# Kernel optimization log

Measured on AMD Instinct MI355X. Metric: run time of the kernel, lower is better.

The kernel has to match this reference:

```python
import jax, jax.numpy as jnp
import numpy as np

D_MODEL = 1024
N_HEADS = 16
DFF = 4096
B, S = 2, 2048
EPS = 1e-6


def _dense_params(key, d_in, d_out):
    kw, kb = jax.random.split(key)
    w = jax.random.normal(kw, (d_in, d_out), jnp.float32) * 0.02
    b = jax.random.normal(kb, (d_out,), jnp.float32) * 0.02
    return w, b


def setup_inputs() -> dict:
    key = jax.random.key(0)
    ks = jax.random.split(key, 20)
    inp = {
        "x": jax.random.normal(ks[0], (B, S, D_MODEL), jnp.float32),
        "enc_output": jax.random.normal(ks[1], (B, S, D_MODEL), jnp.float32),
        # causal look-ahead mask: 1 where attention is NOT allowed
        "look_ahead_mask": jnp.triu(jnp.ones((S, S), jnp.float32), k=1)[None, None],
        "padding_mask": (jax.random.uniform(ks[2], (B, 1, 1, S)) < 0.1).astype(jnp.float32),
    }
    names = ["mha1_wq", "mha1_wk", "mha1_wv", "mha1_wo",
             "mha2_wq", "mha2_wk", "mha2_wv", "mha2_wo"]
    for i, n in enumerate(names):
        w, b = _dense_params(ks[3 + i], D_MODEL, D_MODEL)
        inp[n] = w
        inp[n.replace("w", "b")] = b
    inp["ffn_w1"], inp["ffn_b1"] = _dense_params(ks[11], D_MODEL, DFF)
    inp["ffn_w2"], inp["ffn_b2"] = _dense_params(ks[12], DFF, D_MODEL)
    for i, n in enumerate(["ln1", "ln2", "ln3"]):
        inp[n + "_g"] = jnp.ones((D_MODEL,), jnp.float32)
        inp[n + "_b"] = jnp.zeros((D_MODEL,), jnp.float32)
    return inp


def _layernorm(x, g, b):
    mu = jnp.mean(x, axis=-1, keepdims=True)
    var = jnp.mean(jnp.square(x - mu), axis=-1, keepdims=True)
    return (x - mu) * jax.lax.rsqrt(var + EPS) * g + b


def _mha(v, k, q, mask, wq, bq, wk, bk, wv, bv, wo, bo):
    Bq, Sq, D = q.shape
    depth = D // N_HEADS

    def split(t):  # [B,S,D] -> [B,H,S,depth]
        return t.reshape(t.shape[0], -1, N_HEADS, depth).transpose(0, 2, 1, 3)

    qh = split(q @ wq + bq)
    kh = split(k @ wk + bk)
    vh = split(v @ wv + bv)
    logits = jnp.einsum("bhqd,bhkd->bhqk", qh, kh) / jnp.sqrt(jnp.float32(depth))
    if mask is not None:
        logits = logits + mask * (-1e9)
    attn = jax.nn.softmax(logits, axis=-1)
    out = jnp.einsum("bhqk,bhkd->bhqd", attn, vh)
    out = out.transpose(0, 2, 1, 3).reshape(Bq, Sq, D)
    return out @ wo + bo


def reference(x, enc_output, look_ahead_mask, padding_mask,
              mha1_wq, mha1_bq, mha1_wk, mha1_bk, mha1_wv, mha1_bv, mha1_wo, mha1_bo,
              mha2_wq, mha2_bq, mha2_wk, mha2_bk, mha2_wv, mha2_bv, mha2_wo, mha2_bo,
              ffn_w1, ffn_b1, ffn_w2, ffn_b2,
              ln1_g, ln1_b, ln2_g, ln2_b, ln3_g, ln3_b):
    # self-attention (training=False -> dropout is identity)
    attn1 = _mha(x, x, x, look_ahead_mask,
                 mha1_wq, mha1_bq, mha1_wk, mha1_bk, mha1_wv, mha1_bv, mha1_wo, mha1_bo)
    out1 = _layernorm(x + attn1, ln1_g, ln1_b)
    # cross-attention: q from decoder, k/v from encoder output
    attn2 = _mha(enc_output, enc_output, out1, padding_mask,
                 mha2_wq, mha2_bq, mha2_wk, mha2_bk, mha2_wv, mha2_bv, mha2_wo, mha2_bo)
    out2 = _layernorm(out1 + attn2, ln2_g, ln2_b)
    ffn = jax.nn.relu(out2 @ ffn_w1 + ffn_b1) @ ffn_w2 + ffn_b2
    return _layernorm(out2 + ffn, ln3_g, ln3_b)
```

## Files before the change

### kernel.cpp

```cpp
#include <hip/hip_runtime.h>
#include <hip/hip_bf16.h>
#include <stdint.h>

#define DM   1024
#define NH   16
#define SS   2048
#define BB   2
#define MT   4096

typedef __attribute__((ext_vector_type(8))) short short8;
typedef __attribute__((ext_vector_type(4))) float f32x4;

typedef __attribute__((address_space(1))) const unsigned int as1_uint;
typedef __attribute__((address_space(3))) unsigned int as3_uint;

__device__ __forceinline__ void async16(const void* g, void* l) {
  __builtin_amdgcn_global_load_lds((as1_uint*)g, (as3_uint*)l, 16, 0, 0);
}

#define WAITV(n) asm volatile("s_waitcnt vmcnt(" #n ")" ::: "memory")
#define BARRIER_SB() do { __builtin_amdgcn_s_barrier(); __builtin_amdgcn_sched_barrier(0); } while (0)
#define EXP2(x) __builtin_amdgcn_exp2f(x)

__device__ __forceinline__ unsigned short f2bf(float f) {
  union { float f; unsigned u; } c; c.f = f;
  unsigned r = c.u + 0x7fffu + ((c.u >> 16) & 1u);
  return (unsigned short)(r >> 16);
}

__device__ __forceinline__ unsigned cvt_pk_bf16(float lo, float hi) {
  unsigned r;
  asm("v_cvt_pk_bf16_f32 %0, %1, %2" : "=v"(r) : "v"(lo), "v"(hi));
  return r;
}

__device__ __forceinline__ float swz16(float x) {
  return __uint_as_float((unsigned)__builtin_amdgcn_ds_swizzle((int)__float_as_uint(x), 0x401F));
}

__global__ __launch_bounds__(256) void k_f32_to_bf16(
    const float* __restrict__ in, unsigned short* __restrict__ out, int n) {
  int i = (blockIdx.x * 256 + threadIdx.x) * 4;
  if (i >= n) return;
  float4 v = *(const float4*)(in + i);
  uint2 u;
  u.x = (unsigned)f2bf(v.x) | ((unsigned)f2bf(v.y) << 16);
  u.y = (unsigned)f2bf(v.z) | ((unsigned)f2bf(v.w) << 16);
  *(uint2*)(out + i) = u;
}

__global__ __launch_bounds__(256) void k_transpose_bf16(
    const float* __restrict__ in, unsigned short* __restrict__ out, int R, int C) {
  __shared__ float t[64][65];
  int c0 = blockIdx.x * 64, r0 = blockIdx.y * 64;
  int tx = threadIdx.x & 63, ty = threadIdx.x >> 6;
#pragma unroll
  for (int i = 0; i < 16; i++)
    t[ty + i * 4][tx] = in[(size_t)(r0 + ty + i * 4) * C + c0 + tx];
  __syncthreads();
#pragma unroll
  for (int i = 0; i < 16; i++)
    out[(size_t)(c0 + ty + i * 4) * R + r0 + tx] = f2bf(t[tx][ty + i * 4]);
}

template<int BM, int OUT_MODE, bool RELU, bool RESID, bool SPLITK>
__global__ __launch_bounds__(256) void k_gemm(
    const unsigned short* __restrict__ A,
    const unsigned short* __restrict__ Bt,
    const float* __restrict__ bias,
    const float* __restrict__ resid,
    void* __restrict__ outp, void* __restrict__ outp2,
    int M, int N, int K, int KS) {
  __shared__ unsigned short Alds[3][BM * 32];
  __shared__ unsigned short Blds[3][128 * 32];
  int tid = threadIdx.x;
  int w = tid >> 6, lane = tid & 63;
  int l15 = lane & 15, l4 = lane >> 4;
  int brow = blockIdx.y * BM, bcol = blockIdx.x * 128;

  constexpr int MR = 4;
  constexpr int NR = (BM == 128) ? 4 : 2;
  int wr = (BM == 128) ? (w >> 1) : 0;
  int wc = (BM == 128) ? (w & 1) : w;
  int rbase = wr * 64;
  int cbase = wc * (NR * 16);

  f32x4 acc[MR][NR];
#pragma unroll
  for (int i = 0; i < MR; i++)
#pragma unroll
    for (int j = 0; j < NR; j++) acc[i][j] = (f32x4){0.f, 0.f, 0.f, 0.f};

#define STAGEG(bufi, kk) do {                                                  \
    _Pragma("unroll")                                                          \
    for (int c = 0; c < BM / 64; c++) {                                        \
      int elem = (c * 256 + tid) * 8;                                          \
      int row = elem >> 5, col = elem & 31;                                    \
      async16(A + (size_t)(brow + row) * K + (kk) + col, &Alds[bufi][elem]);   \
    }                                                                          \
    _Pragma("unroll")                                                          \
    for (int c = 0; c < 2; c++) {                                              \
      int elem = (c * 256 + tid) * 8;                                          \
      int row = elem >> 5, col = elem & 31;                                    \
      async16(Bt + (size_t)(bcol + row) * K + (kk) + col, &Blds[bufi][elem]);  \
    } } while (0)

  int kbeg = SPLITK ? blockIdx.z * KS : 0;
  int nk = KS / 32;
  STAGEG(0, kbeg);
  if (nk > 1) {
    STAGEG(1, kbeg + 32);
    if (BM == 128) WAITV(4); else WAITV(3);
  } else {
    WAITV(0);
  }
  BARRIER_SB();

  for (int t = 0; t < nk; t++) {
    int buf = t % 3;
    if (t + 2 < nk) STAGEG((t + 2) % 3, kbeg + (t + 2) * 32);
    short8 af[MR], bfr[NR];
#pragma unroll
    for (int i = 0; i < MR; i++)
      af[i] = *(const short8*)&Alds[buf][(rbase + i * 16 + l15) * 32 + l4 * 8];
#pragma unroll
    for (int j = 0; j < NR; j++)
      bfr[j] = *(const short8*)&Blds[buf][(cbase + j * 16 + l15) * 32 + l4 * 8];
#pragma unroll
    for (int i = 0; i < MR; i++)
#pragma unroll
      for (int j = 0; j < NR; j++)
        acc[i][j] = __builtin_amdgcn_mfma_f32_16x16x32_bf16(af[i], bfr[j], acc[i][j], 0, 0, 0);
    if (t + 2 < nk) {
      if (BM == 128) WAITV(4); else WAITV(3);
    } else if (t + 1 < nk) {
      WAITV(0);
    }
    if (t + 1 < nk) BARRIER_SB();
  }
#undef STAGEG

  void* op = (SPLITK && blockIdx.z) ? outp2 : outp;
#pragma unroll
  for (int i = 0; i < MR; i++)
#pragma unroll
    for (int j = 0; j < NR; j++) {
      int row = brow + rbase + i * 16 + l4 * 4;
      int col = bcol + cbase + j * 16 + l15;
      float bs = (SPLITK || !bias) ? 0.f : bias[col];
#pragma unroll
      for (int r = 0; r < 4; r++) {
        float v = acc[i][j][r] + bs;
        if (RESID) v += resid[(size_t)(row + r) * N + col];
        if (RELU) v = fmaxf(v, 0.f);
        if (OUT_MODE == 0) ((float*)op)[(size_t)(row + r) * N + col] = v;
        else               ((unsigned short*)op)[(size_t)(row + r) * N + col] = f2bf(v);
      }
    }
}

__global__ __launch_bounds__(256) void k_gemm_qkv(
    const unsigned short* __restrict__ a0, const unsigned short* __restrict__ a1,
    const unsigned short* __restrict__ a2,
    const unsigned short* __restrict__ Bt,
    const float* __restrict__ b0, const float* __restrict__ b1, const float* __restrict__ b2,
    unsigned short* __restrict__ o0, unsigned short* __restrict__ o1, unsigned short* __restrict__ o2,
    int vmat, int M, int K) {
  __shared__ unsigned short Alds[3][128 * 32];
  __shared__ unsigned short Blds[3][128 * 32];
  int tid = threadIdx.x;
  int w = tid >> 6, lane = tid & 63;
  int wr = w >> 1, wc = w & 1;
  int l15 = lane & 15, l4 = lane >> 4;
  int z = blockIdx.z;
  const unsigned short* A  = (z == 0) ? a0 : (z == 1) ? a1 : a2;
  const unsigned short* Bz = Bt + (size_t)z * 1048576;
  int brow = blockIdx.y * 128, bcol = blockIdx.x * 128;

  f32x4 acc[4][4];
#pragma unroll
  for (int i = 0; i < 4; i++)
#pragma unroll
    for (int j = 0; j < 4; j++) acc[i][j] = (f32x4){0.f, 0.f, 0.f, 0.f};

#define STAGEQ(bufi, kk) do {                                                  \
    _Pragma("unroll")                                                          \
    for (int c = 0; c < 2; c++) {                                              \
      int elem = (c * 256 + tid) * 8;                                          \
      int row = elem >> 5, col = elem & 31;                                    \
      async16(A + (size_t)(brow + row) * K + (kk) + col, &Alds[bufi][elem]);   \
      async16(Bz + (size_t)(bcol + row) * K + (kk) + col, &Blds[bufi][elem]);  \
    } } while (0)

  int nk = K / 32;
  STAGEQ(0, 0);
  STAGEQ(1, 32);
  WAITV(4);
  BARRIER_SB();

  for (int t = 0; t < nk; t++) {
    int buf = t % 3;
    if (t + 2 < nk) STAGEQ((t + 2) % 3, (t + 2) * 32);
    short8 af[4], bfr[4];
#pragma unroll
    for (int i = 0; i < 4; i++) {
      af[i]  = *(const short8*)&Alds[buf][(wr * 64 + i * 16 + l15) * 32 + l4 * 8];
      bfr[i] = *(const short8*)&Blds[buf][(wc * 64 + i * 16 + l15) * 32 + l4 * 8];
    }
#pragma unroll
    for (int i = 0; i < 4; i++)
#pragma unroll
      for (int j = 0; j < 4; j++)
        acc[i][j] = __builtin_amdgcn_mfma_f32_16x16x32_bf16(af[i], bfr[j], acc[i][j], 0, 0, 0);
    if (t + 2 < nk) WAITV(4);
    else if (t + 1 < nk) WAITV(0);
    if (t + 1 < nk) BARRIER_SB();
  }
#undef STAGEQ

  const float* bias = (z == 0) ? b0 : (z == 1) ? b1 : b2;
  unsigned short* op = (z == 0) ? o0 : (z == 1) ? o1 : o2;
  bool tr = (z == vmat);
#pragma unroll
  for (int i = 0; i < 4; i++)
#pragma unroll
    for (int j = 0; j < 4; j++) {
      int row = brow + wr * 64 + i * 16 + l4 * 4;
      int colL = bcol + wc * 64 + j * 16 + l15;
      float bs = bias[colL];
#pragma unroll
      for (int r = 0; r < 4; r++) {
        float v = acc[i][j][r] + bs;
        if (tr) op[(size_t)colL * M + row + r] = f2bf(v);
        else    op[(size_t)(row + r) * 1024 + colL] = f2bf(v);
      }
    }
}

template<bool CAUSAL, int NF>
__global__ __launch_bounds__(256) void k_attn(
    const unsigned short* __restrict__ Q,
    const unsigned short* __restrict__ Kb,
    const unsigned short* __restrict__ Vt,
    const float* __restrict__ pm,
    unsigned short* __restrict__ out) {
  __shared__ unsigned short Klds[3][64 * 64];
  __shared__ unsigned short Vlds[3][64 * 64];
  __shared__ unsigned short Pw[4][NF][16 * 72];
  int tid = threadIdx.x, w = tid >> 6, lane = tid & 63;
  int l15 = lane & 15, l4 = lane >> 4;
  int h = blockIdx.y, b = blockIdx.z;
  const float SC = 0.125f * 1.44269504089f;
  const int NPASS = CAUSAL ? 2 : 1;

#define STAGE(bufi, kt_) do {                                                  \
    _Pragma("unroll")                                                          \
    for (int c = 0; c < 2; c++) {                                              \
      int e0 = w * 1024 + c * 512;                                             \
      int elem = e0 + lane * 8;                                                \
      int row_ = elem >> 6;                                                    \
      int col_ = (elem & 63) ^ ((row_ & 7) << 3);                              \
      async16(Kb + (size_t)(b * SS + (kt_) * 64 + row_) * DM + h * 64 + col_,  \
              &Klds[bufi][elem]);                                              \
      async16(Vt + (size_t)(h * 64 + row_) * MT + b * SS + (kt_) * 64 + col_,  \
              &Vlds[bufi][elem]);                                              \
    } } while (0)

  for (int pass = 0; pass < NPASS; pass++) {
    int qt = CAUSAL ? (pass == 0 ? (31 - (int)blockIdx.x) : (int)blockIdx.x)
                    : (int)blockIdx.x;
    int qbase = qt * (NF * 64) + w * (NF * 16);

    short8 qf[NF][2];
#pragma unroll
    for (int f = 0; f < NF; f++) {
      size_t qrow = (size_t)b * SS + qbase + f * 16 + l15;
#pragma unroll
      for (int ks = 0; ks < 2; ks++)
        qf[f][ks] = *(const short8*)(Q + qrow * DM + h * 64 + ks * 32 + l4 * 8);
    }

    float mrow[NF], lrow[NF];
    f32x4 accO[NF][4];
#pragma unroll
    for (int f = 0; f < NF; f++) {
      mrow[f] = -1e30f; lrow[f] = 0.f;
#pragma unroll
      for (int d = 0; d < 4; d++) accO[f][d] = (f32x4){0.f, 0.f, 0.f, 0.f};
    }

    int ktend = CAUSAL ? qt : (SS / 64 - 1);
    if (pass) BARRIER_SB();
    STAGE(0, 0);
    if (ktend >= 1) { STAGE(1, 1); WAITV(4); } else { WAITV(0); }
    BARRIER_SB();

    for (int kt = 0; kt <= ktend; kt++) {
      int buf = kt % 3;
      if (kt + 2 <= ktend) STAGE((kt + 2) % 3, kt + 2);

      bool active = !CAUSAL || (kt * 64 <= qbase + NF * 16 - 1);
      if (active) {
        f32x4 sa[NF][4];
#pragma unroll
        for (int f = 0; f < NF; f++)
#pragma unroll
          for (int nt = 0; nt < 4; nt++) sa[f][nt] = (f32x4){0.f, 0.f, 0.f, 0.f};
        __builtin_amdgcn_s_setprio(1);
#pragma unroll
        for (int ks = 0; ks < 2; ks++)
#pragma unroll
          for (int nt = 0; nt < 4; nt++) {
            int kr = nt * 16 + l15;
            short8 kf = *(const short8*)&Klds[buf][kr * 64 + ((ks * 32 + l4 * 8) ^ ((kr & 7) << 3))];
#pragma unroll
            for (int f = 0; f < NF; f++)
              sa[f][nt] = __builtin_amdgcn_mfma_f32_16x16x32_bf16(kf, qf[f][ks], sa[f][nt], 0, 0, 0);
          }
        __builtin_amdgcn_s_setprio(0);

        float pmb[16];
        if (!CAUSAL) {
#pragma unroll
          for (int nt = 0; nt < 4; nt++) {
            float4 pmv = *(const float4*)(pm + b * SS + kt * 64 + nt * 16 + l4 * 4);
#pragma unroll
            for (int r = 0; r < 4; r++) pmb[nt * 4 + r] = ((const float*)&pmv)[r] * -1e30f;
          }
        }
        bool diag = CAUSAL && (kt * 64 + 63 > qbase);

        float sv[NF][16], tm[NF];
#pragma unroll
        for (int f = 0; f < NF; f++) {
          if (CAUSAL && !diag) {
#pragma unroll
            for (int i = 0; i < 16; i++) sv[f][i] = sa[f][i >> 2][i & 3] * SC;
          } else if (CAUSAL) {
#pragma unroll
            for (int nt = 0; nt < 4; nt++)
#pragma unroll
              for (int r = 0; r < 4; r++) {
                float s = sa[f][nt][r] * SC;
                int kg = kt * 64 + nt * 16 + l4 * 4 + r;
                int qg = qbase + f * 16 + l15;
                if (kg > qg) s = -1e30f;
                sv[f][nt * 4 + r] = s;
              }
          } else {
#pragma unroll
            for (int i = 0; i < 16; i++)
              sv[f][i] = fmaf(sa[f][i >> 2][i & 3], SC, pmb[i]);
          }
          float t8[8];
#pragma unroll
          for (int i = 0; i < 8; i++) t8[i] = fmaxf(sv[f][i], sv[f][i + 8]);
#pragma unroll
          for (int i = 0; i < 4; i++) t8[i] = fmaxf(t8[i], t8[i + 4]);
          t8[0] = fmaxf(t8[0], t8[1]);
          t8[2] = fmaxf(t8[2], t8[3]);
          tm[f] = fmaxf(t8[0], t8[2]);
        }

        float sA[NF];
#pragma unroll
        for (int f = 0; f < NF; f++) sA[f] = swz16(tm[f]);
#pragma unroll
        for (int f = 0; f < NF; f++) tm[f] = fmaxf(tm[f], sA[f]);
        float xA[NF];
#pragma unroll
        for (int f = 0; f < NF; f++) xA[f] = __shfl_xor(tm[f], 32);
#pragma unroll
        for (int f = 0; f < NF; f++) tm[f] = fmaxf(tm[f], xA[f]);

#pragma unroll
        for (int f = 0; f < NF; f++) {
          if (!__all(tm[f] - mrow[f] <= 8.f)) {
            float mnew = fmaxf(mrow[f], tm[f]);
            float corr = EXP2(mrow[f] - mnew);
            mrow[f] = mnew;
            lrow[f] *= corr;
#pragma unroll
            for (int r = 0; r < 4; r++) {
              float cq = __shfl(corr, l4 * 4 + r);
#pragma unroll
              for (int dt = 0; dt < 4; dt++) accO[f][dt][r] *= cq;
            }
          }

          float p[16];
#pragma unroll
          for (int i = 0; i < 16; i++) p[i] = EXP2(sv[f][i] - mrow[f]);
          float a8[8];
#pragma unroll
          for (int i = 0; i < 8; i++) a8[i] = p[i] + p[i + 8];
#pragma unroll
          for (int i = 0; i < 4; i++) a8[i] = a8[i] + a8[i + 4];
          lrow[f] += (a8[0] + a8[1]) + (a8[2] + a8[3]);

#pragma unroll
          for (int nt = 0; nt < 4; nt++) {
            uint2 u;
            u.x = cvt_pk_bf16(p[nt * 4 + 0], p[nt * 4 + 1]);
            u.y = cvt_pk_bf16(p[nt * 4 + 2], p[nt * 4 + 3]);
            *(uint2*)&Pw[w][f][l15 * 72 + nt * 16 + l4 * 4] = u;
          }
        }

        __builtin_amdgcn_s_setprio(1);
#pragma unroll
        for (int ks = 0; ks < 2; ks++) {
          short8 pf[NF];
#pragma unroll
          for (int f = 0; f < NF; f++)
            pf[f] = *(const short8*)&Pw[w][f][l15 * 72 + ks * 32 + l4 * 8];
#pragma unroll
          for (int dt = 0; dt < 4; dt++) {
            int vr = dt * 16 + l15;
            short8 vf = *(const short8*)&Vlds[buf][vr * 64 + ((ks * 32 + l4 * 8) ^ ((vr & 7) << 3))];
#pragma unroll
            for (int f = 0; f < NF; f++)
              accO[f][dt] = __builtin_amdgcn_mfma_f32_16x16x32_bf16(pf[f], vf, accO[f][dt], 0, 0, 0);
          }
        }
        __builtin_amdgcn_s_setprio(0);
      }

      if (kt + 2 <= ktend) WAITV(4);
      else if (kt + 1 <= ktend) WAITV(0);
      if (kt + 1 <= ktend) BARRIER_SB();
    }

#pragma unroll
    for (int f = 0; f < NF; f++) {
      lrow[f] += swz16(lrow[f]);
      lrow[f] += __shfl_xor(lrow[f], 32);
    }
#pragma unroll
    for (int f = 0; f < NF; f++)
#pragma unroll
      for (int r = 0; r < 4; r++) {
        float lq = __shfl(lrow[f], l4 * 4 + r);
        float inv = 1.f / lq;
        size_t row = (size_t)b * SS + qbase + f * 16 + l4 * 4 + r;
#pragma unroll
        for (int dt = 0; dt < 4; dt++)
          out[row * DM + h * 64 + dt * 16 + l15] = f2bf(accO[f][dt][r] * inv);
      }
  }
#undef STAGE
}

__global__ __launch_bounds__(256) void k_ln(
    const float* __restrict__ in, const float* __restrict__ in2,
    const float* __restrict__ resid, const float* __restrict__ bias,
    const float* __restrict__ g, const float* __restrict__ bb,
    float* __restrict__ outf, unsigned short* __restrict__ outb) {
  int row = blockIdx.x, tid = threadIdx.x;
  int w = tid >> 6;
  __shared__ float red[4];
  float4 v = *(const float4*)(in + (size_t)row * 1024 + tid * 4);
  if (in2) {
    float4 v2 = *(const float4*)(in2 + (size_t)row * 1024 + tid * 4);
    v.x += v2.x; v.y += v2.y; v.z += v2.z; v.w += v2.w;
  }
  if (resid) {
    float4 v2 = *(const float4*)(resid + (size_t)row * 1024 + tid * 4);
    v.x += v2.x; v.y += v2.y; v.z += v2.z; v.w += v2.w;
  }
  if (bias) {
    float4 v2 = *(const float4*)(bias + tid * 4);
    v.x += v2.x; v.y += v2.y; v.z += v2.z; v.w += v2.w;
  }
  float s = v.x + v.y + v.z + v.w;
#pragma unroll
  for (int d = 1; d < 64; d <<= 1) s += __shfl_xor(s, d);
  if ((tid & 63) == 0) red[w] = s;
  __syncthreads();
  float mu = (red[0] + red[1] + red[2] + red[3]) * (1.f / 1024.f);
  float d0 = v.x - mu, d1 = v.y - mu, d2 = v.z - mu, d3 = v.w - mu;
  float q = d0 * d0 + d1 * d1 + d2 * d2 + d3 * d3;
#pragma unroll
  for (int d = 1; d < 64; d <<= 1) q += __shfl_xor(q, d);
  __syncthreads();
  if ((tid & 63) == 0) red[w] = q;
  __syncthreads();
  float var = (red[0] + red[1] + red[2] + red[3]) * (1.f / 1024.f);
  float rs = rsqrtf(var + 1e-6f);
  float4 gg = *(const float4*)(g + tid * 4);
  float4 bv = *(const float4*)(bb + tid * 4);
  float y0 = d0 * rs * gg.x + bv.x;
  float y1 = d1 * rs * gg.y + bv.y;
  float y2 = d2 * rs * gg.z + bv.z;
  float y3 = d3 * rs * gg.w + bv.w;
  if (outf) {
    float4 o; o.x = y0; o.y = y1; o.z = y2; o.w = y3;
    *(float4*)(outf + (size_t)row * 1024 + tid * 4) = o;
  }
  if (outb) {
    uint2 u;
    u.x = (unsigned)f2bf(y0) | ((unsigned)f2bf(y1) << 16);
    u.y = (unsigned)f2bf(y2) | ((unsigned)f2bf(y3) << 16);
    *(uint2*)(outb + (size_t)row * 1024 + tid * 4) = u;
  }
}

extern "C" void kernel_launch(void* const* d_in, const int* in_sizes, int n_in,
                              void* d_out, int out_size, void* d_ws, size_t ws_size,
                              hipStream_t stream) {
  const float* x    = (const float*)d_in[0];
  const float* enc  = (const float*)d_in[1];
  const float* pm   = (const float*)d_in[3];
  const float* wq1  = (const float*)d_in[4];   const float* bq1 = (const float*)d_in[5];
  const float* wk1  = (const float*)d_in[6];   const float* bk1 = (const float*)d_in[7];
  const float* wv1  = (const float*)d_in[8];   const float* bv1 = (const float*)d_in[9];
  const float* wo1  = (const float*)d_in[10];  const float* bo1 = (const float*)d_in[11];
  const float* wq2  = (const float*)d_in[12];  const float* bq2 = (const float*)d_in[13];
  const float* wk2  = (const float*)d_in[14];  const float* bk2 = (const float*)d_in[15];
  const float* wv2  = (const float*)d_in[16];  const float* bv2 = (const float*)d_in[17];
  const float* wo2  = (const float*)d_in[18];  const float* bo2 = (const float*)d_in[19];
  const float* fw1  = (const float*)d_in[20];  const float* fb1 = (const float*)d_in[21];
  const float* fw2  = (const float*)d_in[22];  const float* fb2 = (const float*)d_in[23];
  const float* ln1g = (const float*)d_in[24];  const float* ln1b = (const float*)d_in[25];
  const float* ln2g = (const float*)d_in[26];  const float* ln2b = (const float*)d_in[27];
  const float* ln3g = (const float*)d_in[28];  const float* ln3b = (const float*)d_in[29];

  char* ws = (char*)d_ws;
  unsigned short* XB = (unsigned short*)(ws + 0);
  unsigned short* EB = (unsigned short*)(ws + 8388608);
  unsigned short* Qb = (unsigned short*)(ws + 16777216);
  unsigned short* Kb = (unsigned short*)(ws + 25165824);
  unsigned short* Vt = (unsigned short*)(ws + 33554432);
  unsigned short* AT = (unsigned short*)(ws + 41943040);
  float*          T  = (float*)(ws + 50331648);
  float*          R  = (float*)(ws + 67108864);
  unsigned short* RB = (unsigned short*)(ws + 83886080);
  unsigned short* WT0 = (unsigned short*)(ws + 92274688);
  unsigned short* W1T = (unsigned short*)(ws + 92274688 + 16777216);
  unsigned short* W2T = (unsigned short*)(ws + 92274688 + 25165824);
  unsigned short* H   = (unsigned short*)(ws + 0);
  float*          T1  = (float*)(ws + 33554432);
  float*          T1o = (float*)(ws + 16777216);

  k_f32_to_bf16<<<4096, 256, 0, stream>>>(x, XB, MT * DM);
  k_f32_to_bf16<<<4096, 256, 0, stream>>>(enc, EB, MT * DM);
  const float* wlist[8] = {wq1, wk1, wv1, wo1, wq2, wk2, wv2, wo2};
  for (int i = 0; i < 8; i++)
    k_transpose_bf16<<<dim3(16, 16), 256, 0, stream>>>(wlist[i], WT0 + (size_t)i * 1048576, 1024, 1024);
  k_transpose_bf16<<<dim3(64, 16), 256, 0, stream>>>(fw1, W1T, 1024, 4096);
  k_transpose_bf16<<<dim3(16, 64), 256, 0, stream>>>(fw2, W2T, 4096, 1024);

  k_gemm_qkv<<<dim3(8, 32, 3), 256, 0, stream>>>(XB, XB, XB, WT0, bq1, bk1, bv1,
                                                 Qb, Kb, Vt, 2, MT, DM);
  k_attn<true, 1><<<dim3(16, 16, 2), 256, 0, stream>>>(Qb, Kb, Vt, nullptr, AT);
  k_gemm<64, 0, false, false, true><<<dim3(8, 64, 2), 256, 0, stream>>>(
      AT, WT0 + 3 * 1048576, nullptr, nullptr, T, T1o, MT, DM, DM, 512);
  k_ln<<<4096, 256, 0, stream>>>(T, T1o, x, bo1, ln1g, ln1b, R, RB);

  k_gemm_qkv<<<dim3(8, 32, 3), 256, 0, stream>>>(RB, EB, EB, WT0 + 4 * 1048576,
                                                 bq2, bk2, bv2, Qb, Kb, Vt, 2, MT, DM);
  k_attn<false, 2><<<dim3(16, 16, 2), 256, 0, stream>>>(Qb, Kb, Vt, pm, AT);
  k_gemm<64, 0, false, false, true><<<dim3(8, 64, 2), 256, 0, stream>>>(
      AT, WT0 + 7 * 1048576, nullptr, nullptr, T, T1o, MT, DM, DM, 512);
  k_ln<<<4096, 256, 0, stream>>>(T, T1o, R, bo2, ln2g, ln2b, R, RB);

  k_gemm<128, 1, true, false, false><<<dim3(32, 32), 256, 0, stream>>>(
      RB, W1T, fb1, nullptr, H, nullptr, MT, 4096, DM, 1024);
  k_gemm<64, 0, false, false, true><<<dim3(8, 64, 2), 256, 0, stream>>>(
      H, W2T, nullptr, nullptr, T, T1, MT, DM, 4096, 2048);
  k_ln<<<4096, 256, 0, stream>>>(T, T1, R, fb2, ln3g, ln3b, (float*)d_out, nullptr);
}
```

Baseline: 450.6 us.

## Batch conversion/transpose launches and add XCD-aware block swizzle to GEMMs

```diff
diff --git a/kernel.cpp b/kernel.cpp
--- a/kernel.cpp
+++ b/kernel.cpp
@@ -38,10 +38,24 @@
   return __uint_as_float((unsigned)__builtin_amdgcn_ds_swizzle((int)__float_as_uint(x), 0x401F));
 }
 
-__global__ __launch_bounds__(256) void k_f32_to_bf16(
-    const float* __restrict__ in, unsigned short* __restrict__ out, int n) {
-  int i = (blockIdx.x * 256 + threadIdx.x) * 4;
-  if (i >= n) return;
+__device__ __forceinline__ void xcd_swz(int& bx, int& by, int& bz) {
+  int GX = gridDim.x, GY = gridDim.y;
+  int nwg = GX * GY * gridDim.z;
+  int old = blockIdx.x + GX * (blockIdx.y + GY * blockIdx.z);
+  int f2 = (old & 7) * (nwg >> 3) + (old >> 3);
+  bz = f2 / (GX * GY);
+  int rem = f2 % (GX * GY);
+  bx = rem / GY;
+  by = rem % GY;
+}
+
+__global__ __launch_bounds__(256) void k_conv2(
+    const float* __restrict__ a, const float* __restrict__ b,
+    unsigned short* __restrict__ oa, unsigned short* __restrict__ ob) {
+  int bxr = blockIdx.x;
+  const float* in = (bxr < 4096) ? a : b;
+  unsigned short* out = (bxr < 4096) ? oa : ob;
+  int i = ((bxr & 4095) * 256 + threadIdx.x) * 4;
   float4 v = *(const float4*)(in + i);
   uint2 u;
   u.x = (unsigned)f2bf(v.x) | ((unsigned)f2bf(v.y) << 16);
@@ -61,6 +75,23 @@
 #pragma unroll
   for (int i = 0; i < 16; i++)
     out[(size_t)(c0 + ty + i * 4) * R + r0 + tx] = f2bf(t[tx][ty + i * 4]);
+}
+
+struct PtrArr { const float* p[8]; };
+__global__ __launch_bounds__(256) void k_transpose8(
+    PtrArr ps, unsigned short* __restrict__ out0) {
+  __shared__ float t[64][65];
+  const float* in = ps.p[blockIdx.z];
+  unsigned short* out = out0 + (size_t)blockIdx.z * 1048576;
+  int c0 = blockIdx.x * 64, r0 = blockIdx.y * 64;
+  int tx = threadIdx.x & 63, ty = threadIdx.x >> 6;
+#pragma unroll
+  for (int i = 0; i < 16; i++)
+    t[ty + i * 4][tx] = in[(size_t)(r0 + ty + i * 4) * 1024 + c0 + tx];
+  __syncthreads();
+#pragma unroll
+  for (int i = 0; i < 16; i++)
+    out[(size_t)(c0 + ty + i * 4) * 1024 + r0 + tx] = f2bf(t[tx][ty + i * 4]);
 }
 
 template<int BM, int OUT_MODE, bool RELU, bool RESID, bool SPLITK>
@@ -76,7 +107,9 @@
   int tid = threadIdx.x;
   int w = tid >> 6, lane = tid & 63;
   int l15 = lane & 15, l4 = lane >> 4;
-  int brow = blockIdx.y * BM, bcol = blockIdx.x * 128;
+  int bxs, bys, bzs;
+  xcd_swz(bxs, bys, bzs);
+  int brow = bys * BM, bcol = bxs * 128;
 
   constexpr int MR = 4;
   constexpr int NR = (BM == 128) ? 4 : 2;
@@ -105,7 +138,7 @@
       async16(Bt + (size_t)(bcol + row) * K + (kk) + col, &Blds[bufi][elem]);  \
     } } while (0)
 
-  int kbeg = SPLITK ? blockIdx.z * KS : 0;
+  int kbeg = SPLITK ? bzs * KS : 0;
   int nk = KS / 32;
   STAGEG(0, kbeg);
   if (nk > 1) {
@@ -140,7 +173,7 @@
   }
 #undef STAGEG
 
-  void* op = (SPLITK && blockIdx.z) ? outp2 : outp;
+  void* op = (SPLITK && bzs) ? outp2 : outp;
 #pragma unroll
   for (int i = 0; i < MR; i++)
 #pragma unroll
@@ -172,10 +205,11 @@
   int w = tid >> 6, lane = tid & 63;
   int wr = w >> 1, wc = w & 1;
   int l15 = lane & 15, l4 = lane >> 4;
-  int z = blockIdx.z;
+  int bxs, bys, z;
+  xcd_swz(bxs, bys, z);
   const unsigned short* A  = (z == 0) ? a0 : (z == 1) ? a1 : a2;
   const unsigned short* Bz = Bt + (size_t)z * 1048576;
-  int brow = blockIdx.y * 128, bcol = blockIdx.x * 128;
+  int brow = bys * 128, bcol = bxs * 128;
 
   f32x4 acc[4][4];
 #pragma unroll
@@ -542,11 +576,11 @@
   float*          T1  = (float*)(ws + 33554432);
   float*          T1o = (float*)(ws + 16777216);
 
-  k_f32_to_bf16<<<4096, 256, 0, stream>>>(x, XB, MT * DM);
-  k_f32_to_bf16<<<4096, 256, 0, stream>>>(enc, EB, MT * DM);
-  const float* wlist[8] = {wq1, wk1, wv1, wo1, wq2, wk2, wv2, wo2};
-  for (int i = 0; i < 8; i++)
-    k_transpose_bf16<<<dim3(16, 16), 256, 0, stream>>>(wlist[i], WT0 + (size_t)i * 1048576, 1024, 1024);
+  k_conv2<<<8192, 256, 0, stream>>>(x, enc, XB, EB);
+  PtrArr ptrs;
+  ptrs.p[0] = wq1; ptrs.p[1] = wk1; ptrs.p[2] = wv1; ptrs.p[3] = wo1;
+  ptrs.p[4] = wq2; ptrs.p[5] = wk2; ptrs.p[6] = wv2; ptrs.p[7] = wo2;
+  k_transpose8<<<dim3(16, 16, 8), 256, 0, stream>>>(ptrs, WT0);
   k_transpose_bf16<<<dim3(64, 16), 256, 0, stream>>>(fw1, W1T, 1024, 4096);
   k_transpose_bf16<<<dim3(16, 64), 256, 0, stream>>>(fw2, W2T, 4096, 1024);
 
```

After: 452.9 us. About the same (+0.5%).
